# Optimization experiments

Measured on AMD Instinct MI355X. Metric: run time of the kernel, lower is better.

The kernel has to match this reference:

```python
import jax, jax.numpy as jnp
import numpy as np
from jax import lax

EPS = 1e-5
K = 7
G = 4


def _dwconv_bn(x, w, g, b, m, v):
    # depthwise 3x3, pad 1, then BN (eval mode with running stats)
    C = x.shape[1]
    y = lax.conv_general_dilated(x, w, (1, 1), [(1, 1), (1, 1)],
                                 feature_group_count=C,
                                 dimension_numbers=('NCHW', 'OIHW', 'NCHW'))
    scale = (g / jnp.sqrt(v + EPS))[None, :, None, None]
    return (y - m[None, :, None, None]) * scale + b[None, :, None, None]


def _proj(t, pw1, pb1, pw2, pb2):
    # 1x1 conv -> GELU(exact) -> 1x1 conv, on small spatial maps
    h = jnp.einsum('bchw,oc->bohw', t, pw1) + pb1[None, :, None, None]
    h = jax.nn.gelu(h, approximate=False)
    return jnp.einsum('bchw,oc->bohw', h, pw2) + pb2[None, :, None, None]


def setup_inputs() -> dict:
    key = jax.random.key(0)
    ks = jax.random.split(key, 17)
    B, C, H, W = 16, 256, 56, 56
    r = C // 4
    inp = {
        'x1': jax.random.normal(ks[0], (B, C, H, W), jnp.float32),
        'dw1_w': jax.random.normal(ks[1], (C, 1, 3, 3), jnp.float32) * 0.1,
        'dw1_g': jax.random.uniform(ks[2], (C,), jnp.float32, 0.5, 1.5),
        'dw1_b': jax.random.normal(ks[3], (C,), jnp.float32) * 0.1,
        'dw1_m': jax.random.normal(ks[4], (C,), jnp.float32) * 0.1,
        'dw1_v': jax.random.uniform(ks[5], (C,), jnp.float32, 0.5, 1.5),
        'dw2_w': jax.random.normal(ks[6], (C, 1, 3, 3), jnp.float32) * 0.1,
        'dw2_g': jax.random.uniform(ks[7], (C,), jnp.float32, 0.5, 1.5),
        'dw2_b': jax.random.normal(ks[8], (C,), jnp.float32) * 0.1,
        'dw2_m': jax.random.normal(ks[9], (C,), jnp.float32) * 0.1,
        'dw2_v': jax.random.uniform(ks[10], (C,), jnp.float32, 0.5, 1.5),
        'weight1': jax.random.normal(ks[11], (G, C, K, K), jnp.float32) * 0.02,
        'bias1': jax.random.normal(ks[12], (G, C), jnp.float32) * 0.02,
        'pw1': jax.random.normal(ks[13], (r, C), jnp.float32) * 0.05,
        'pb1': jax.random.normal(ks[14], (r,), jnp.float32) * 0.05,
        'pw2': jax.random.normal(ks[15], (C * G, r), jnp.float32) * 0.05,
        'pb2': jax.random.normal(ks[16], (C * G,), jnp.float32) * 0.05,
    }
    return inp


def reference(x1, dw1_w, dw1_g, dw1_b, dw1_m, dw1_v,
              dw2_w, dw2_g, dw2_b, dw2_m, dw2_v,
              weight1, bias1, pw1, pb1, pw2, pb2):
    B, C, H, W = x1.shape
    # gated fuse: relu6(dw1(x)) * dw2(x)
    a = jnp.clip(_dwconv_bn(x1, dw1_w, dw1_g, dw1_b, dw1_m, dw1_v), 0.0, 6.0)
    x_fuse = a * _dwconv_bn(x1, dw2_w, dw2_g, dw2_b, dw2_m, dw2_v)

    # adaptive avg pool to (K,K): H,W multiples of K -> uniform block means
    pooled = x_fuse.reshape(B, C, K, H // K, K, W // K).mean(axis=(3, 5))

    # dynamic kernel: proj -> softmax over groups -> weighted sum of weight1
    scale1 = _proj(pooled, pw1, pb1, pw2, pb2).reshape(B, G, C, K, K)
    scale1 = jax.nn.softmax(scale1, axis=1)
    w_dyn = jnp.sum(scale1 * weight1[None], axis=1)  # [B, C, K, K]

    # dynamic bias
    mean_x = x_fuse.mean(axis=(-2, -1), keepdims=True)  # [B, C, 1, 1]
    sb = _proj(mean_x, pw1, pb1, pw2, pb2).reshape(B, G, C)
    sb = jax.nn.softmax(sb, axis=1)
    b_dyn = jnp.sum(sb * bias1[None], axis=1)  # [B, C]

    # per-sample depthwise conv with dynamic weights
    pad = K // 2

    def per_sample(xi, wi):  # xi [C,H,W], wi [C,K,K]
        y = lax.conv_general_dilated(xi[None], wi[:, None], (1, 1),
                                     [(pad, pad), (pad, pad)],
                                     feature_group_count=C,
                                     dimension_numbers=('NCHW', 'OIHW', 'NCHW'))
        return y[0]

    out = jax.vmap(per_sample)(x_fuse, w_dyn)  # [B, C, H, W]
    return out + b_dyn[:, :, None, None]
```

## Files before the change

### kernel.cpp

```cpp
#include <hip/hip_runtime.h>
#include <math.h>

#define BATCH 16
#define CH 256
#define HW 56
#define NPIX (HW*HW)

__device__ __forceinline__ void fuse_tile(
    const float* __restrict__ plane, int ty, int tx,
    const float w1[9], const float w2[9],
    float sc1, float be1, float sc2, float be2,
    float res[4][4])
{
    const int oy = 4 * ty;
    float y1a[4][4], y2a[4][4];
    #pragma unroll
    for (int a = 0; a < 4; a++)
        #pragma unroll
        for (int e = 0; e < 4; e++) { y1a[a][e] = 0.f; y2a[a][e] = 0.f; }

    #pragma unroll
    for (int iy = 0; iy < 6; iy++) {
        const int r    = oy - 1 + iy;
        const bool rok = (r >= 0) && (r < 56);
        const int rc   = rok ? r : 0;
        float rb[12];
        #pragma unroll
        for (int k = 0; k < 3; k++) {
            const int cx  = tx - 1 + k;
            const bool cv = (cx >= 0) && (cx < 14);
            const int cc2 = cv ? cx : 0;
            const bool ok = rok && cv;
            float4 v = *(const float4*)(plane + rc*56 + 4*cc2);
            rb[4*k+0] = ok ? v.x : 0.f;
            rb[4*k+1] = ok ? v.y : 0.f;
            rb[4*k+2] = ok ? v.z : 0.f;
            rb[4*k+3] = ok ? v.w : 0.f;
        }
        #pragma unroll
        for (int tyy = 0; tyy < 4; tyy++) {
            const int ky = iy - tyy;
            if (ky >= 0 && ky < 3) {
                #pragma unroll
                for (int e = 0; e < 4; e++)
                    #pragma unroll
                    for (int dj = 0; dj < 3; dj++) {
                        float xv = rb[3 + e + dj];
                        y1a[tyy][e] += xv * w1[ky*3+dj];
                        y2a[tyy][e] += xv * w2[ky*3+dj];
                    }
            }
        }
    }
    #pragma unroll
    for (int tyy = 0; tyy < 4; tyy++)
        #pragma unroll
        for (int e = 0; e < 4; e++) {
            float y1 = y1a[tyy][e] * sc1 + be1;
            float y2 = y2a[tyy][e] * sc2 + be2;
            float a = fminf(fmaxf(y1, 0.f), 6.f);
            res[tyy][e] = a * y2;
        }
}

__global__ __launch_bounds__(256) void k1_pool(
    const float* __restrict__ x1,
    const float* __restrict__ dw1w, const float* __restrict__ g1, const float* __restrict__ b1,
    const float* __restrict__ m1, const float* __restrict__ v1,
    const float* __restrict__ dw2w, const float* __restrict__ g2, const float* __restrict__ b2,
    const float* __restrict__ m2, const float* __restrict__ v2,
    float* __restrict__ pooled)
{
    const int bc = blockIdx.x;
    const int c  = bc & 255;
    const int t  = threadIdx.x;

    __shared__ float part[196];

    float w1[9], w2[9];
    #pragma unroll
    for (int k = 0; k < 9; k++) { w1[k] = dw1w[c*9+k]; w2[k] = dw2w[c*9+k]; }
    const float sc1 = g1[c] * rsqrtf(v1[c] + 1e-5f);
    const float be1 = b1[c] - m1[c] * sc1;
    const float sc2 = g2[c] * rsqrtf(v2[c] + 1e-5f);
    const float be2 = b2[c] - m2[c] * sc2;

    if (t < 196) {
        const int ty = t / 14, tx = t - ty * 14;
        float res[4][4];
        fuse_tile(x1 + (size_t)bc * NPIX, ty, tx, w1, w2, sc1, be1, sc2, be2, res);
        float s = 0.f;
        #pragma unroll
        for (int a = 0; a < 4; a++)
            #pragma unroll
            for (int e = 0; e < 4; e++) s += res[a][e];
        part[t] = s;
    }
    __syncthreads();
    if (t < 49) {
        int ph = t / 7, pw = t - ph * 7;
        float s = part[(2*ph  )*14 + 2*pw] + part[(2*ph  )*14 + 2*pw + 1]
                + part[(2*ph+1)*14 + 2*pw] + part[(2*ph+1)*14 + 2*pw + 1];
        pooled[(size_t)bc * 49 + t] = s * (1.f/64.f);
    }
}

__global__ __launch_bounds__(256) void k2a(
    const float* __restrict__ pooled, const float* __restrict__ pw1,
    const float* __restrict__ pb1, float* __restrict__ h)
{
    const int b  = blockIdx.x;
    const int oc = blockIdx.y;
    const int t  = threadIdx.x;
    __shared__ float pl[256*50];

    const float* pp = pooled + (size_t)b * 256 * 49;
    for (int idx = t; idx < 256*49; idx += 256) {
        int cc = idx / 49, p = idx - cc * 49;
        pl[cc*50 + p] = pp[idx];
    }
    __syncthreads();
    {
        float s = 0.f;
        #pragma unroll
        for (int p = 0; p < 49; p++) s += pl[t*50 + p];
        pl[t*50 + 49] = s * (1.f/49.f);
    }
    __syncthreads();

    for (int idx = t; idx < 16*50; idx += 256) {
        int ol = idx / 50, p = idx - ol * 50;
        int o = oc * 16 + ol;
        const float* wrow = pw1 + o * 256;
        float acc = pb1[o];
        #pragma unroll 8
        for (int cc = 0; cc < 256; cc++) acc += wrow[cc] * pl[cc*50 + p];
        float gv = 0.5f * acc * (1.f + erff(acc * 0.70710678118654752f));
        h[((size_t)b * 50 + p) * 64 + o] = gv;
    }
}

__global__ __launch_bounds__(256) void k2b(
    const float* __restrict__ h, const float* __restrict__ pw2, const float* __restrict__ pb2,
    const float* __restrict__ weight1, const float* __restrict__ bias1,
    float* __restrict__ w_dyn, float* __restrict__ b_dyn)
{
    const int b   = blockIdx.x;
    const int cch = blockIdx.y;
    const int t   = threadIdx.x;
    const int c_base = cch * 16;

    __shared__ __attribute__((aligned(16))) float hl[50*64];
    __shared__ float sl[64*51];

    const float* hp = h + (size_t)b * 50 * 64;
    for (int i = t; i < 800; i += 256) ((float4*)hl)[i] = ((const float4*)hp)[i];

    const int row = t & 63;
    const int pb  = t >> 6;
    const int g   = row >> 4, cl = row & 15;
    const int o2  = (g << 8) + c_base + cl;

    float wreg[64];
    {
        const float4* w4 = (const float4*)(pw2 + (size_t)o2 * 64);
        #pragma unroll
        for (int r4 = 0; r4 < 16; r4++) {
            float4 v = w4[r4];
            wreg[4*r4] = v.x; wreg[4*r4+1] = v.y; wreg[4*r4+2] = v.z; wreg[4*r4+3] = v.w;
        }
    }
    const float bias2 = pb2[o2];
    __syncthreads();

    for (int p = pb; p < 50; p += 4) {
        const float4* hv = (const float4*)&hl[p*64];
        float acc = bias2;
        #pragma unroll
        for (int r4 = 0; r4 < 16; r4++) {
            float4 v = hv[r4];
            acc += wreg[4*r4]*v.x + wreg[4*r4+1]*v.y + wreg[4*r4+2]*v.z + wreg[4*r4+3]*v.w;
        }
        sl[row*51 + p] = acc;
    }
    __syncthreads();

    for (int idx = t; idx < 16*50; idx += 256) {
        int cl2 = idx / 50, p = idx - cl2 * 50;
        float s0 = sl[(cl2     )*51 + p];
        float s1 = sl[(16 + cl2)*51 + p];
        float s2 = sl[(32 + cl2)*51 + p];
        float s3 = sl[(48 + cl2)*51 + p];
        float mx = fmaxf(fmaxf(s0, s1), fmaxf(s2, s3));
        float e0 = expf(s0-mx), e1 = expf(s1-mx), e2 = expf(s2-mx), e3 = expf(s3-mx);
        float inv = 1.f / (e0+e1+e2+e3);
        e0 *= inv; e1 *= inv; e2 *= inv; e3 *= inv;
        int cc = c_base + cl2;
        if (p < 49) {
            float wv = e0*weight1[(0*256+cc)*49+p] + e1*weight1[(1*256+cc)*49+p]
                     + e2*weight1[(2*256+cc)*49+p] + e3*weight1[(3*256+cc)*49+p];
            w_dyn[((size_t)b*256 + cc)*49 + p] = wv;
        } else {
            b_dyn[b*256 + cc] = e0*bias1[cc] + e1*bias1[256+cc] + e2*bias1[512+cc] + e3*bias1[768+cc];
        }
    }
}

#define S3 68
__global__ __launch_bounds__(256) void k3_dyn(
    const float* __restrict__ x1,
    const float* __restrict__ dw1w, const float* __restrict__ g1, const float* __restrict__ b1,
    const float* __restrict__ m1, const float* __restrict__ v1,
    const float* __restrict__ dw2w, const float* __restrict__ g2, const float* __restrict__ b2,
    const float* __restrict__ m2, const float* __restrict__ v2,
    const float* __restrict__ w_dyn, const float* __restrict__ b_dyn,
    float* __restrict__ out)
{
    const int bc = blockIdx.x;
    const int c  = bc & 255;
    const int t  = threadIdx.x;
    __shared__ __attribute__((aligned(16))) float halo[62*S3];

    float w1[9], w2[9];
    #pragma unroll
    for (int k = 0; k < 9; k++) { w1[k] = dw1w[c*9+k]; w2[k] = dw2w[c*9+k]; }
    const float sc1 = g1[c] * rsqrtf(v1[c] + 1e-5f);
    const float be1 = b1[c] - m1[c] * sc1;
    const float sc2 = g2[c] * rsqrtf(v2[c] + 1e-5f);
    const float be2 = b2[c] - m2[c] * sc2;
    float wk[49];
    const float* wp = w_dyn + (size_t)bc * 49;
    #pragma unroll
    for (int k = 0; k < 49; k++) wk[k] = wp[k];
    const float bias = b_dyn[bc];

    {
        float4 z = make_float4(0.f, 0.f, 0.f, 0.f);
        float4* h4 = (float4*)halo;
        for (int i = t; i < 62*S3/4; i += 256) h4[i] = z;
    }
    __syncthreads();

    const int ty = t / 14, tx = t - ty * 14;
    if (t < 196) {
        float res[4][4];
        fuse_tile(x1 + (size_t)bc * NPIX, ty, tx, w1, w2, sc1, be1, sc2, be2, res);
        #pragma unroll
        for (int tyy = 0; tyy < 4; tyy++) {
            float4 r4; r4.x=res[tyy][0]; r4.y=res[tyy][1]; r4.z=res[tyy][2]; r4.w=res[tyy][3];
            *(float4*)&halo[(4*ty + tyy + 3)*S3 + 4 + 4*tx] = r4;
        }
    }
    __syncthreads();

    if (t < 196) {
        const int oy = ty * 4, ox = tx * 4;
        float acc[4][4];
        #pragma unroll
        for (int a = 0; a < 4; a++)
            #pragma unroll
            for (int bb = 0; bb < 4; bb++) acc[a][bb] = bias;

        #pragma unroll
        for (int iy = 0; iy < 10; iy++) {
            const float* hr = &halo[(oy+iy)*S3 + ox];
            float4 a = *(const float4*)hr;
            float4 b = *(const float4*)(hr + 4);
            float4 cc = *(const float4*)(hr + 8);
            float row[12];
            row[0]=a.x; row[1]=a.y; row[2]=a.z; row[3]=a.w;
            row[4]=b.x; row[5]=b.y; row[6]=b.z; row[7]=b.w;
            row[8]=cc.x; row[9]=cc.y; row[10]=cc.z; row[11]=cc.w;
            #pragma unroll
            for (int tyy = 0; tyy < 4; tyy++) {
                const int ky = iy - tyy;
                if (ky >= 0 && ky < 7) {
                    #pragma unroll
                    for (int txx = 0; txx < 4; txx++)
                        #pragma unroll
                        for (int kx = 0; kx < 7; kx++)
                            acc[tyy][txx] += row[1+txx+kx] * wk[ky*7+kx];
                }
            }
        }
        float* op = out + (size_t)bc * NPIX;
        #pragma unroll
        for (int tyy = 0; tyy < 4; tyy++) {
            float4 r4; r4.x = acc[tyy][0]; r4.y = acc[tyy][1]; r4.z = acc[tyy][2]; r4.w = acc[tyy][3];
            *(float4*)(op + (oy+tyy)*56 + ox) = r4;
        }
    }
}

extern "C" void kernel_launch(void* const* d_in, const int* in_sizes, int n_in,
                              void* d_out, int out_size, void* d_ws, size_t ws_size,
                              hipStream_t stream) {
    const float* x1    = (const float*)d_in[0];
    const float* dw1w  = (const float*)d_in[1];
    const float* dw1g  = (const float*)d_in[2];
    const float* dw1b  = (const float*)d_in[3];
    const float* dw1m  = (const float*)d_in[4];
    const float* dw1v  = (const float*)d_in[5];
    const float* dw2w  = (const float*)d_in[6];
    const float* dw2g  = (const float*)d_in[7];
    const float* dw2b  = (const float*)d_in[8];
    const float* dw2m  = (const float*)d_in[9];
    const float* dw2v  = (const float*)d_in[10];
    const float* weight1 = (const float*)d_in[11];
    const float* bias1   = (const float*)d_in[12];
    const float* pw1     = (const float*)d_in[13];
    const float* pb1     = (const float*)d_in[14];
    const float* pw2     = (const float*)d_in[15];
    const float* pb2     = (const float*)d_in[16];

    float* out = (float*)d_out;
    float* ws  = (float*)d_ws;
    float* pooled = ws;
    float* h      = ws + 200704;
    float* w_dyn  = ws + 251904;
    float* b_dyn  = ws + 452608;

    k1_pool<<<BATCH*CH, 256, 0, stream>>>(x1, dw1w, dw1g, dw1b, dw1m, dw1v,
                                          dw2w, dw2g, dw2b, dw2m, dw2v, pooled);
    k2a<<<dim3(BATCH, 4), 256, 0, stream>>>(pooled, pw1, pb1, h);
    k2b<<<dim3(BATCH, 16), 256, 0, stream>>>(h, pw2, pb2, weight1, bias1, w_dyn, b_dyn);
    k3_dyn<<<BATCH*CH, 256, 0, stream>>>(x1, dw1w, dw1g, dw1b, dw1m, dw1v,
                                         dw2w, dw2g, dw2b, dw2m, dw2v,
                                         w_dyn, b_dyn, out);
}
```

Before: 201.2 us.

## Map pool kernel to one thread per 8x8 cell and balance dynamic conv warps

The pooling kernel now gives each thread a whole 8x8 pooling cell. It computes the fused depthwise/BN/ReLU6 product with a rolling three-row register window and writes the pooled mean directly, with no shared memory or block sync. This packs all 256 threads of each block with work where the old version left 60 idle. In the dynamic conv kernel, the first three waves do the 4x4 tiles while the fourth wave zeroes only the halo border and computes the last 64 pixels one per thread. This removes the full-halo zero pass and its extra barrier, at the cost of a scalar, divergent tail path.

```diff
diff --git a/kernel.cpp b/kernel.cpp
--- a/kernel.cpp
+++ b/kernel.cpp
@@ -63,7 +63,23 @@
         }
 }
 
-__global__ __launch_bounds__(256) void k1_pool(
+#define K1_LOAD_ROW(r, dst) do {                                                 \
+    const int   rr_  = (r);                                                      \
+    const bool  rok_ = ((unsigned)rr_ < 56u);                                    \
+    const float* rp_ = plane + (rok_ ? rr_ : 0) * 56;                            \
+    float4 a_ = *(const float4*)(rp_ + col0);                                    \
+    float4 b_ = *(const float4*)(rp_ + cbase + 4);                               \
+    float4 c_ = *(const float4*)(rp_ + cbase + 8);                               \
+    float4 d_ = *(const float4*)(rp_ + col3);                                    \
+    const bool l_ = rok_ && (cx > 0);                                            \
+    const bool r_ = rok_ && (cx < 6);                                            \
+    (dst)[0]=l_?a_.x:0.f;  (dst)[1]=l_?a_.y:0.f;  (dst)[2]=l_?a_.z:0.f;  (dst)[3]=l_?a_.w:0.f;   \
+    (dst)[4]=rok_?b_.x:0.f;(dst)[5]=rok_?b_.y:0.f;(dst)[6]=rok_?b_.z:0.f;(dst)[7]=rok_?b_.w:0.f; \
+    (dst)[8]=rok_?c_.x:0.f;(dst)[9]=rok_?c_.y:0.f;(dst)[10]=rok_?c_.z:0.f;(dst)[11]=rok_?c_.w:0.f;\
+    (dst)[12]=r_?d_.x:0.f; (dst)[13]=r_?d_.y:0.f; (dst)[14]=r_?d_.z:0.f; (dst)[15]=r_?d_.w:0.f; \
+} while (0)
+
+__global__ __launch_bounds__(256) void k1_cell(
     const float* __restrict__ x1,
     const float* __restrict__ dw1w, const float* __restrict__ g1, const float* __restrict__ b1,
     const float* __restrict__ m1, const float* __restrict__ v1,
@@ -71,11 +87,12 @@
     const float* __restrict__ m2, const float* __restrict__ v2,
     float* __restrict__ pooled)
 {
-    const int bc = blockIdx.x;
-    const int c  = bc & 255;
-    const int t  = threadIdx.x;
-
-    __shared__ float part[196];
+    const int g    = blockIdx.x * 256 + threadIdx.x;
+    const int bc   = g / 49;
+    const int cell = g - bc * 49;
+    const int c    = bc & 255;
+    const int cy   = cell / 7, cx = cell - cy * 7;
+    const float* plane = x1 + (size_t)bc * NPIX;
 
     float w1[9], w2[9];
     #pragma unroll
@@ -85,24 +102,41 @@
     const float sc2 = g2[c] * rsqrtf(v2[c] + 1e-5f);
     const float be2 = b2[c] - m2[c] * sc2;
 
-    if (t < 196) {
-        const int ty = t / 14, tx = t - ty * 14;
-        float res[4][4];
-        fuse_tile(x1 + (size_t)bc * NPIX, ty, tx, w1, w2, sc1, be1, sc2, be2, res);
-        float s = 0.f;
-        #pragma unroll
-        for (int a = 0; a < 4; a++)
+    const int rbase = 8*cy - 1;
+    const int cbase = 8*cx - 4;
+    const int col0  = (cx > 0) ? cbase      : 0;
+    const int col3  = (cx < 6) ? cbase + 12 : 0;
+
+    float rows[3][16];
+    K1_LOAD_ROW(rbase + 0, rows[0]);
+    K1_LOAD_ROW(rbase + 1, rows[1]);
+
+    float sum = 0.f;
+    #pragma unroll
+    for (int yy = 0; yy < 8; yy++) {
+        K1_LOAD_ROW(rbase + yy + 2, rows[(yy + 2) % 3]);
+        float y1[8], y2[8];
+        #pragma unroll
+        for (int e = 0; e < 8; e++) { y1[e] = 0.f; y2[e] = 0.f; }
+        #pragma unroll
+        for (int ky = 0; ky < 3; ky++) {
+            const float* rr = rows[(yy + ky) % 3];
             #pragma unroll
-            for (int e = 0; e < 4; e++) s += res[a][e];
-        part[t] = s;
-    }
-    __syncthreads();
-    if (t < 49) {
-        int ph = t / 7, pw = t - ph * 7;
-        float s = part[(2*ph  )*14 + 2*pw] + part[(2*ph  )*14 + 2*pw + 1]
-                + part[(2*ph+1)*14 + 2*pw] + part[(2*ph+1)*14 + 2*pw + 1];
-        pooled[(size_t)bc * 49 + t] = s * (1.f/64.f);
-    }
+            for (int e = 0; e < 8; e++)
+                #pragma unroll
+                for (int kx = 0; kx < 3; kx++) {
+                    float xv = rr[3 + e + kx];
+                    y1[e] += xv * w1[ky*3+kx];
+                    y2[e] += xv * w2[ky*3+kx];
+                }
+        }
+        #pragma unroll
+        for (int e = 0; e < 8; e++) {
+            float a = fminf(fmaxf(y1[e]*sc1 + be1, 0.f), 6.f);
+            sum += a * (y2[e]*sc2 + be2);
+        }
+    }
+    pooled[(size_t)bc * 49 + cell] = sum * (1.f/64.f);
 }
 
 __global__ __launch_bounds__(256) void k2a(
@@ -233,27 +267,52 @@
     #pragma unroll
     for (int k = 0; k < 49; k++) wk[k] = wp[k];
     const float bias = b_dyn[bc];
-
-    {
-        float4 z = make_float4(0.f, 0.f, 0.f, 0.f);
-        float4* h4 = (float4*)halo;
-        for (int i = t; i < 62*S3/4; i += 256) h4[i] = z;
-    }
-    __syncthreads();
+    const float* plane = x1 + (size_t)bc * NPIX;
 
     const int ty = t / 14, tx = t - ty * 14;
-    if (t < 196) {
+
+    if (t < 192) {
         float res[4][4];
-        fuse_tile(x1 + (size_t)bc * NPIX, ty, tx, w1, w2, sc1, be1, sc2, be2, res);
+        fuse_tile(plane, ty, tx, w1, w2, sc1, be1, sc2, be2, res);
         #pragma unroll
         for (int tyy = 0; tyy < 4; tyy++) {
             float4 r4; r4.x=res[tyy][0]; r4.y=res[tyy][1]; r4.z=res[tyy][2]; r4.w=res[tyy][3];
             *(float4*)&halo[(4*ty + tyy + 3)*S3 + 4 + 4*tx] = r4;
         }
+    } else {
+        const int lane = t - 192;
+        float4 z = make_float4(0.f, 0.f, 0.f, 0.f);
+        for (int task = lane; task < 208; task += 64) {
+            int row, c4;
+            if (task < 96) { int tr = task >> 4; row = (tr < 3) ? tr : 56 + tr; c4 = task & 15; }
+            else           { int m = task - 96;  row = 3 + (m >> 1); c4 = (m & 1) ? 15 : 0; }
+            *(float4*)&halo[row*S3 + 4*c4] = z;
+        }
+        const int tt = lane >> 4;
+        const int p  = lane & 15;
+        const int y  = 52 + (p >> 2);
+        const int x  = 4*(10 + tt) + (p & 3);
+        float y1 = 0.f, y2 = 0.f;
+        #pragma unroll
+        for (int ky = 0; ky < 3; ky++) {
+            const int r  = y - 1 + ky;
+            const bool rv = (r < 56);
+            const int rc = rv ? r : 55;
+            #pragma unroll
+            for (int kx = 0; kx < 3; kx++) {
+                const int cc2 = x - 1 + kx;
+                const bool cv = (cc2 < 56);
+                const float xv = (rv && cv) ? plane[rc*56 + (cv ? cc2 : 55)] : 0.f;
+                y1 += xv * w1[ky*3+kx];
+                y2 += xv * w2[ky*3+kx];
+            }
+        }
+        float a = fminf(fmaxf(y1*sc1 + be1, 0.f), 6.f);
+        halo[(y + 3)*S3 + 4 + x] = a * (y2*sc2 + be2);
     }
     __syncthreads();
 
-    if (t < 196) {
+    if (t < 192) {
         const int oy = ty * 4, ox = tx * 4;
         float acc[4][4];
         #pragma unroll
@@ -289,6 +348,19 @@
             float4 r4; r4.x = acc[tyy][0]; r4.y = acc[tyy][1]; r4.z = acc[tyy][2]; r4.w = acc[tyy][3];
             *(float4*)(op + (oy+tyy)*56 + ox) = r4;
         }
+    } else {
+        const int lane = t - 192;
+        const int tt = lane >> 4;
+        const int p  = lane & 15;
+        const int y  = 52 + (p >> 2);
+        const int x  = 4*(10 + tt) + (p & 3);
+        float acc = bias;
+        #pragma unroll
+        for (int ky = 0; ky < 7; ky++)
+            #pragma unroll
+            for (int kx = 0; kx < 7; kx++)
+                acc += halo[(y + ky)*S3 + (x + 1) + kx] * wk[ky*7+kx];
+        out[(size_t)bc * NPIX + y*56 + x] = acc;
     }
 }
 
@@ -320,8 +392,8 @@
     float* w_dyn  = ws + 251904;
     float* b_dyn  = ws + 452608;
 
-    k1_pool<<<BATCH*CH, 256, 0, stream>>>(x1, dw1w, dw1g, dw1b, dw1m, dw1v,
-                                          dw2w, dw2g, dw2b, dw2m, dw2v, pooled);
+    k1_cell<<<784, 256, 0, stream>>>(x1, dw1w, dw1g, dw1b, dw1m, dw1v,
+                                     dw2w, dw2g, dw2b, dw2m, dw2v, pooled);
     k2a<<<dim3(BATCH, 4), 256, 0, stream>>>(pooled, pw1, pb1, h);
     k2b<<<dim3(BATCH, 16), 256, 0, stream>>>(h, pw2, pb2, weight1, bias1, w_dyn, b_dyn);
     k3_dyn<<<BATCH*CH, 256, 0, stream>>>(x1, dw1w, dw1g, dw1b, dw1m, dw1v,
```

Measured after the change: 204.2 us. About the same (+1.5%).

## Transpose pooled layout and re-parallelize projection kernels across more blocks

Applied to the files above, without the earlier changes.

The pooled output is stored position-major with channels contiguous, so the first projection kernel can run one block per (batch, position), 800 blocks instead of 64. Each output channel's dot product is split across four lanes with float4 loads and a shuffle reduction. The second projection kernel transposes h and pw2 into shared memory so each thread computes all four group logits for one (channel, position) and applies the softmax directly, removing the intermediate logit buffer and one barrier. The intent is to cut latency in the small projection stage, which used too few blocks; the cost is a strided scatter store in the pool kernel and a recomputed channel mean over 49 positions in the per-batch mean block.

```diff
diff --git a/kernel.cpp b/kernel.cpp
--- a/kernel.cpp
+++ b/kernel.cpp
@@ -73,6 +73,7 @@
 {
     const int bc = blockIdx.x;
     const int c  = bc & 255;
+    const int b  = bc >> 8;
     const int t  = threadIdx.x;
 
     __shared__ float part[196];
@@ -101,107 +102,108 @@
         int ph = t / 7, pw = t - ph * 7;
         float s = part[(2*ph  )*14 + 2*pw] + part[(2*ph  )*14 + 2*pw + 1]
                 + part[(2*ph+1)*14 + 2*pw] + part[(2*ph+1)*14 + 2*pw + 1];
-        pooled[(size_t)bc * 49 + t] = s * (1.f/64.f);
+        pooled[((size_t)(b * 50 + t)) * 256 + c] = s * (1.f/64.f);
     }
 }
 
 __global__ __launch_bounds__(256) void k2a(
-    const float* __restrict__ pooled, const float* __restrict__ pw1,
-    const float* __restrict__ pb1, float* __restrict__ h)
-{
-    const int b  = blockIdx.x;
-    const int oc = blockIdx.y;
-    const int t  = threadIdx.x;
-    __shared__ float pl[256*50];
-
-    const float* pp = pooled + (size_t)b * 256 * 49;
-    for (int idx = t; idx < 256*49; idx += 256) {
-        int cc = idx / 49, p = idx - cc * 49;
-        pl[cc*50 + p] = pp[idx];
-    }
-    __syncthreads();
-    {
+    const float* __restrict__ pooled,
+    const float* __restrict__ pw1, const float* __restrict__ pb1,
+    float* __restrict__ h)
+{
+    const int blk = blockIdx.x;
+    const int b = blk / 50, p = blk - b * 50;
+    const int t = threadIdx.x;
+
+    __shared__ __attribute__((aligned(16))) float xs[272];
+
+    const float* base = pooled + (size_t)b * 50 * 256;
+    float v;
+    if (p < 49) {
+        v = base[p * 256 + t];
+    } else {
         float s = 0.f;
-        #pragma unroll
-        for (int p = 0; p < 49; p++) s += pl[t*50 + p];
-        pl[t*50 + 49] = s * (1.f/49.f);
-    }
-    __syncthreads();
-
-    for (int idx = t; idx < 16*50; idx += 256) {
-        int ol = idx / 50, p = idx - ol * 50;
-        int o = oc * 16 + ol;
-        const float* wrow = pw1 + o * 256;
-        float acc = pb1[o];
-        #pragma unroll 8
-        for (int cc = 0; cc < 256; cc++) acc += wrow[cc] * pl[cc*50 + p];
-        float gv = 0.5f * acc * (1.f + erff(acc * 0.70710678118654752f));
-        h[((size_t)b * 50 + p) * 64 + o] = gv;
+        #pragma unroll 7
+        for (int q = 0; q < 49; q++) s += base[q * 256 + t];
+        v = s * (1.f/49.f);
+    }
+    xs[t + 4*(t>>6)] = v;
+    __syncthreads();
+
+    const int o = t >> 2, part = t & 3;
+    const float4* w4 = (const float4*)(pw1 + o*256 + part*64);
+    const float4* x4 = (const float4*)(xs + part*68);
+    float acc = 0.f;
+    #pragma unroll
+    for (int i = 0; i < 16; i++) {
+        float4 w = w4[i];
+        float4 x = x4[i];
+        acc += w.x*x.x + w.y*x.y + w.z*x.z + w.w*x.w;
+    }
+    acc += __shfl_xor(acc, 1);
+    acc += __shfl_xor(acc, 2);
+    if (part == 0) {
+        float zv = acc + pb1[o];
+        h[((size_t)b * 50 + p) * 64 + o] = 0.5f * zv * (1.f + erff(zv * 0.70710678118654752f));
     }
 }
 
 __global__ __launch_bounds__(256) void k2b(
     const float* __restrict__ h, const float* __restrict__ pw2, const float* __restrict__ pb2,
     const float* __restrict__ weight1, const float* __restrict__ bias1,
-    float* __restrict__ w_dyn, float* __restrict__ b_dyn)
+    float* __restrict__ w_dyn,
+    float* __restrict__ b_dyn)
 {
     const int b   = blockIdx.x;
     const int cch = blockIdx.y;
     const int t   = threadIdx.x;
     const int c_base = cch * 16;
 
-    __shared__ __attribute__((aligned(16))) float hl[50*64];
-    __shared__ float sl[64*51];
+    __shared__ float ht[64*52];
+    __shared__ __attribute__((aligned(16))) float wg[16*64*4];
 
     const float* hp = h + (size_t)b * 50 * 64;
-    for (int i = t; i < 800; i += 256) ((float4*)hl)[i] = ((const float4*)hp)[i];
-
-    const int row = t & 63;
-    const int pb  = t >> 6;
-    const int g   = row >> 4, cl = row & 15;
-    const int o2  = (g << 8) + c_base + cl;
-
-    float wreg[64];
-    {
-        const float4* w4 = (const float4*)(pw2 + (size_t)o2 * 64);
-        #pragma unroll
-        for (int r4 = 0; r4 < 16; r4++) {
-            float4 v = w4[r4];
-            wreg[4*r4] = v.x; wreg[4*r4+1] = v.y; wreg[4*r4+2] = v.z; wreg[4*r4+3] = v.w;
-        }
-    }
-    const float bias2 = pb2[o2];
-    __syncthreads();
-
-    for (int p = pb; p < 50; p += 4) {
-        const float4* hv = (const float4*)&hl[p*64];
-        float acc = bias2;
-        #pragma unroll
-        for (int r4 = 0; r4 < 16; r4++) {
-            float4 v = hv[r4];
-            acc += wreg[4*r4]*v.x + wreg[4*r4+1]*v.y + wreg[4*r4+2]*v.z + wreg[4*r4+3]*v.w;
-        }
-        sl[row*51 + p] = acc;
-    }
-    __syncthreads();
-
-    for (int idx = t; idx < 16*50; idx += 256) {
-        int cl2 = idx / 50, p = idx - cl2 * 50;
-        float s0 = sl[(cl2     )*51 + p];
-        float s1 = sl[(16 + cl2)*51 + p];
-        float s2 = sl[(32 + cl2)*51 + p];
-        float s3 = sl[(48 + cl2)*51 + p];
+    for (int idx = t; idx < 800; idx += 256) {
+        const int p = idx >> 4, k4 = idx & 15;
+        float4 v = ((const float4*)(hp + p * 64))[k4];
+        ht[(4*k4+0)*52 + p] = v.x;
+        ht[(4*k4+1)*52 + p] = v.y;
+        ht[(4*k4+2)*52 + p] = v.z;
+        ht[(4*k4+3)*52 + p] = v.w;
+    }
+    for (int idx = t; idx < 1024; idx += 256) {
+        const int r = idx >> 4, k4 = idx & 15;
+        const int g = r >> 4, cl = r & 15;
+        const int o2 = (g << 8) + c_base + cl;
+        float4 v = ((const float4*)(pw2 + (size_t)o2 * 64))[k4];
+        wg[((cl*64) + 4*k4+0)*4 + g] = v.x;
+        wg[((cl*64) + 4*k4+1)*4 + g] = v.y;
+        wg[((cl*64) + 4*k4+2)*4 + g] = v.z;
+        wg[((cl*64) + 4*k4+3)*4 + g] = v.w;
+    }
+    __syncthreads();
+
+    for (int idx = t; idx < 800; idx += 256) {
+        const int cl = idx / 50, p = idx - cl * 50;
+        const int c  = c_base + cl;
+        float s0 = pb2[c], s1 = pb2[256 + c], s2 = pb2[512 + c], s3 = pb2[768 + c];
+        const float4* wv = (const float4*)wg + cl * 64;
+        #pragma unroll
+        for (int k = 0; k < 64; k++) {
+            const float x = ht[k*52 + p];
+            const float4 w = wv[k];
+            s0 += x * w.x; s1 += x * w.y; s2 += x * w.z; s3 += x * w.w;
+        }
         float mx = fmaxf(fmaxf(s0, s1), fmaxf(s2, s3));
         float e0 = expf(s0-mx), e1 = expf(s1-mx), e2 = expf(s2-mx), e3 = expf(s3-mx);
         float inv = 1.f / (e0+e1+e2+e3);
         e0 *= inv; e1 *= inv; e2 *= inv; e3 *= inv;
-        int cc = c_base + cl2;
         if (p < 49) {
-            float wv = e0*weight1[(0*256+cc)*49+p] + e1*weight1[(1*256+cc)*49+p]
-                     + e2*weight1[(2*256+cc)*49+p] + e3*weight1[(3*256+cc)*49+p];
-            w_dyn[((size_t)b*256 + cc)*49 + p] = wv;
+            float wvv = e0*weight1[(0*256+c)*49+p] + e1*weight1[(1*256+c)*49+p]
+                      + e2*weight1[(2*256+c)*49+p] + e3*weight1[(3*256+c)*49+p];
+            w_dyn[((size_t)b*256 + c)*49 + p] = wvv;
         } else {
-            b_dyn[b*256 + cc] = e0*bias1[cc] + e1*bias1[256+cc] + e2*bias1[512+cc] + e3*bias1[768+cc];
+            b_dyn[b*256 + c] = e0*bias1[c] + e1*bias1[256+c] + e2*bias1[512+c] + e3*bias1[768+c];
         }
     }
 }
@@ -316,13 +318,13 @@
     float* out = (float*)d_out;
     float* ws  = (float*)d_ws;
     float* pooled = ws;
-    float* h      = ws + 200704;
-    float* w_dyn  = ws + 251904;
-    float* b_dyn  = ws + 452608;
+    float* h      = ws + 204800;
+    float* w_dyn  = ws + 256000;
+    float* b_dyn  = ws + 456704;
 
     k1_pool<<<BATCH*CH, 256, 0, stream>>>(x1, dw1w, dw1g, dw1b, dw1m, dw1v,
                                           dw2w, dw2g, dw2b, dw2m, dw2v, pooled);
-    k2a<<<dim3(BATCH, 4), 256, 0, stream>>>(pooled, pw1, pb1, h);
+    k2a<<<800, 256, 0, stream>>>(pooled, pw1, pb1, h);
     k2b<<<dim3(BATCH, 16), 256, 0, stream>>>(h, pw2, pb2, weight1, bias1, w_dyn, b_dyn);
     k3_dyn<<<BATCH*CH, 256, 0, stream>>>(x1, dw1w, dw1g, dw1b, dw1m, dw1v,
                                          dw2w, dw2g, dw2b, dw2m, dw2v,
```

Result: faster. 191.9 us (-4.6%).
